# Performance work log

Measured on AMD Instinct MI355X. Metric: run time of the kernel, lower is better.

The kernel has to match this reference:

```python
import jax, jax.numpy as jnp
import numpy as np

B, S, IN, OUT = 4, 2048, 4096, 16384

def setup_inputs() -> dict:
    key = jax.random.key(0)
    k1, k2, k3, k4 = jax.random.split(key, 4)
    inp = jax.random.normal(k1, (B, S, IN), dtype=jnp.float16)
    # int8 quantized weights, stored [in_features, out_features] (pre-transposed)
    qweight = jax.random.randint(k2, (IN, OUT), -128, 128, dtype=jnp.int32).astype(jnp.int8)
    # per-output-channel dequant scales, small positive values typical of symmetric quant
    weight_scales = (jax.random.uniform(k3, (OUT,), dtype=jnp.float32) * 0.01 + 0.001).astype(jnp.float16)
    bias = jax.random.normal(k4, (OUT,), dtype=jnp.float16)
    return {"input": inp, "qweight": qweight, "weight_scales": weight_scales, "bias": bias}

def reference(input, qweight, weight_scales, bias):
    # w8_a16_gemm: dequantize int8 weight with per-column scale, then GEMM in fp16
    w = qweight.astype(jnp.float16) * weight_scales[None, :]        # [IN, OUT]
    out = jnp.einsum('bsi,io->bso', input, w)                        # [B, S, OUT]
    return out + bias
```

## Files before the change

### kernel.cpp

```cpp
#include <hip/hip_runtime.h>
#include <stdint.h>


typedef __bf16 bf16x8 __attribute__((ext_vector_type(8)));
typedef float  f32x4  __attribute__((ext_vector_type(4)));

#define M_TOT 8192
#define N_TOT 16384
#define K_TOT 4096
#define BM 256
#define BN 256
#define BK 64
#define NT (K_TOT / BK)
#define SLOT_ELEMS 16384

__device__ __forceinline__ void gload_lds16(const void* g, void* l) {
  __builtin_amdgcn_global_load_lds(
      (const __attribute__((address_space(1))) unsigned int*)g,
      (__attribute__((address_space(3))) unsigned int*)l,
      16, 0, 0);
}

__global__ void __launch_bounds__(256)
prep_kernel(const float* __restrict__ A, __bf16* __restrict__ Abf,
            const int* __restrict__ Q, __bf16* __restrict__ Bt) {
  __shared__ __bf16 t[64][72];
  const int tid = threadIdx.x;
  if (blockIdx.x < 16384) {
    const size_t i = ((size_t)blockIdx.x * 256 + tid) * 8;
    f32x4 lo = *(const f32x4*)(A + i);
    f32x4 hi = *(const f32x4*)(A + i + 4);
    bf16x8 v;
    #pragma unroll
    for (int j = 0; j < 4; ++j) {
      v[j]     = (__bf16)lo[j];
      v[j + 4] = (__bf16)hi[j];
    }
    *(bf16x8*)(Abf + i) = v;
  } else {
    const int bid = blockIdx.x - 16384;
    const int bk = bid & 63;
    const int bn = bid >> 6;
    const int k0 = bk * 64, n0 = bn * 64;
    const int tx = tid & 63;
    const int ty = tid >> 6;
    const int kb = ty * 16;
    int q[16];
    #pragma unroll
    for (int i = 0; i < 16; ++i)
      q[i] = Q[(size_t)(k0 + kb + i) * N_TOT + n0 + tx];
    bf16x8 v0, v1;
    #pragma unroll
    for (int i = 0; i < 8; ++i) {
      v0[i] = (__bf16)(float)q[i];
      v1[i] = (__bf16)(float)q[i + 8];
    }
    *(bf16x8*)&t[tx][kb]     = v0;
    *(bf16x8*)&t[tx][kb + 8] = v1;
    __syncthreads();
    const int nrow = tid >> 2;
    const int kc   = (tid & 3) * 16;
    bf16x8 w0 = *(const bf16x8*)&t[nrow][kc];
    bf16x8 w1 = *(const bf16x8*)&t[nrow][kc + 8];
    __bf16* dst = Bt + (size_t)(n0 + nrow) * K_TOT + k0 + kc;
    *(bf16x8*)(dst)     = w0;
    *(bf16x8*)(dst + 8) = w1;
  }
}

__global__ void __launch_bounds__(512, 2)
w8a16_gemm_ws(const __bf16* __restrict__ A,
              const __bf16* __restrict__ Bt,
              const float*  __restrict__ S,
              const float*  __restrict__ Bias,
              float*        __restrict__ O)
{
  extern __shared__ __bf16 lds[];
  __bf16* const aBase = lds;
  __bf16* const bBase = lds + 3 * SLOT_ELEMS;

  const int tid  = threadIdx.x;
  const int lane = tid & 63;
  const int wv   = tid >> 6;
  const int wm   = wv >> 2;
  const int wn   = wv & 3;
  const int rot  = (wv >> 2) << 1;

  const int bid = blockIdx.x;
  const int xcd = bid & 7;
  const int c   = bid >> 3;
  const int bx  = xcd * 8 + (c >> 5);
  const int by  = c & 31;
  const int m0  = by * BM;
  const int n0  = bx * BN;

  const int rr   = tid >> 3;
  const int cswz = (tid & 7) ^ (rr & 7);
  const __bf16* pa0 = A  + (size_t)(m0 + 0   + rr) * K_TOT + cswz * 8;
  const __bf16* pa1 = A  + (size_t)(m0 + 64  + rr) * K_TOT + cswz * 8;
  const __bf16* pa2 = A  + (size_t)(m0 + 128 + rr) * K_TOT + cswz * 8;
  const __bf16* pa3 = A  + (size_t)(m0 + 192 + rr) * K_TOT + cswz * 8;
  const __bf16* pb0 = Bt + (size_t)(n0 + 0   + rr) * K_TOT + cswz * 8;
  const __bf16* pb1 = Bt + (size_t)(n0 + 64  + rr) * K_TOT + cswz * 8;
  const __bf16* pb2 = Bt + (size_t)(n0 + 128 + rr) * K_TOT + cswz * 8;
  const __bf16* pb3 = Bt + (size_t)(n0 + 192 + rr) * K_TOT + cswz * 8;
  const int dA = tid * 8;

#define STAGE_A(dst) do {                                  \
    gload_lds16(pa0, (dst) + dA);                          \
    gload_lds16(pa1, (dst) + 4096  + dA);                  \
    gload_lds16(pa2, (dst) + 8192  + dA);                  \
    gload_lds16(pa3, (dst) + 12288 + dA);                  \
    pa0 += BK; pa1 += BK; pa2 += BK; pa3 += BK;            \
  } while (0)
#define STAGE_B(dst) do {                                  \
    gload_lds16(pb0, (dst) + dA);                          \
    gload_lds16(pb1, (dst) + 4096  + dA);                  \
    gload_lds16(pb2, (dst) + 8192  + dA);                  \
    gload_lds16(pb3, (dst) + 12288 + dA);                  \
    pb0 += BK; pb1 += BK; pb2 += BK; pb3 += BK;            \
  } while (0)

  const int l15     = lane & 15;
  const int quad    = lane >> 4;
  const int physA0  = quad ^ (l15 & 7);
  const int bRowOff = (wn * 64 + l15) * 64;

  f32x4 acc[8][4];
  #pragma unroll
  for (int i = 0; i < 8; ++i)
    #pragma unroll
    for (int j = 0; j < 4; ++j)
      acc[i][j] = {0.f, 0.f, 0.f, 0.f};

  bf16x8 b0[4][2], b1[4][2];

  STAGE_A(aBase);
  STAGE_B(bBase);
  STAGE_B(bBase + SLOT_ELEMS);
  STAGE_A(aBase + SLOT_ELEMS);
  asm volatile("s_waitcnt vmcnt(4)" ::: "memory");
  __builtin_amdgcn_s_barrier();

  #pragma unroll
  for (int ni = 0; ni < 4; ++ni)
    #pragma unroll
    for (int ks = 0; ks < 2; ++ks)
      b0[ni][ks] = *(const bf16x8*)(
          bBase + bRowOff + ni * 1024 + (physA0 ^ (ks << 2)) * 8);
  asm volatile("s_waitcnt lgkmcnt(0)" ::: "memory");
  __builtin_amdgcn_s_barrier();

  int csA = 0;
  int nsA = 2;

#define TILE_BODY(t, BCUR, BNXT, bStageLds, bReadLds) do {                  \
    if ((t) < NT - 1) { asm volatile("s_waitcnt vmcnt(4)" ::: "memory"); }  \
    else              { asm volatile("s_waitcnt vmcnt(0)" ::: "memory"); }  \
    asm volatile("s_waitcnt lgkmcnt(0)" ::: "memory");                      \
    __builtin_amdgcn_s_barrier();                                           \
    const __bf16* const aC_ = aBase + csA * SLOT_ELEMS;                     \
    __bf16* const aN_ = aBase + nsA * SLOT_ELEMS;                           \
    _Pragma("unroll")                                                       \
    for (int pp = 0; pp < 4; ++pp) {                                        \
      const int qq = (pp + rot) & 3;                                        \
      const __bf16* aQ = aC_ + (wm * 128 + qq * 32 + l15) * 64;             \
      bf16x8 aA[2][2];                                                      \
      _Pragma("unroll")                                                     \
      for (int i = 0; i < 2; ++i)                                           \
        _Pragma("unroll")                                                   \
        for (int ks = 0; ks < 2; ++ks)                                      \
          aA[i][ks] = *(const bf16x8*)(                                     \
              aQ + i * 1024 + (physA0 ^ (ks << 2)) * 8);                    \
      if ((t) + 1 < NT) {                                                   \
        BNXT[pp][0] = *(const bf16x8*)(                                     \
            (bReadLds) + bRowOff + pp * 1024 + physA0 * 8);                 \
        BNXT[pp][1] = *(const bf16x8*)(                                     \
            (bReadLds) + bRowOff + pp * 1024 + (physA0 ^ 4) * 8);           \
      }                                                                     \
      if (pp == 0 && (t) + 2 < NT) STAGE_B(bStageLds);                      \
      if (pp == 1 && (t) + 2 < NT) STAGE_A(aN_);                            \
      __builtin_amdgcn_s_setprio(1);                                        \
      _Pragma("unroll")                                                     \
      for (int i = 0; i < 2; ++i)                                           \
        _Pragma("unroll")                                                   \
        for (int ni = 0; ni < 4; ++ni)                                      \
          _Pragma("unroll")                                                 \
          for (int ks = 0; ks < 2; ++ks)                                    \
            acc[2 * pp + i][ni] = __builtin_amdgcn_mfma_f32_16x16x32_bf16(  \
                aA[i][ks], BCUR[ni][ks], acc[2 * pp + i][ni], 0, 0, 0);     \
      __builtin_amdgcn_s_setprio(0);                                        \
    }                                                                       \
    csA = (csA == 2) ? 0 : csA + 1;                                         \
    nsA = (nsA == 2) ? 0 : nsA + 1;                                         \
  } while (0)

  for (int tt = 0; tt < NT; tt += 2) {
    TILE_BODY(tt,     b0, b1, bBase,              bBase + SLOT_ELEMS);
    TILE_BODY(tt + 1, b1, b0, bBase + SLOT_ELEMS, bBase);
  }
#undef TILE_BODY
#undef STAGE_A
#undef STAGE_B

  const int colb = n0 + wn * 64 + l15;
  #pragma unroll
  for (int pp = 0; pp < 4; ++pp) {
    const int qq = (pp + rot) & 3;
    const int rowq = m0 + wm * 128 + qq * 32 + quad * 4;
    #pragma unroll
    for (int i = 0; i < 2; ++i) {
      const int rowb = rowq + i * 16;
      #pragma unroll
      for (int ni = 0; ni < 4; ++ni) {
        const int col = colb + ni * 16;
        const float sc = S[col];
        const float bb = Bias[col];
        f32x4 a = acc[2 * pp + i][ni];
        #pragma unroll
        for (int j = 0; j < 4; ++j)
          O[(size_t)(rowb + j) * N_TOT + col] = a[j] * sc + bb;
      }
    }
  }
}

#define FBM 128
#define FBN 128
#define FBK 32
#define BSTRIDE 40
__device__ __forceinline__ int swz_s(int row) {
  return (row & 3) ^ ((row >> 2) & 1);
}
__global__ void __launch_bounds__(256)
w8a16_gemm_fused(const float* __restrict__ A, const int* __restrict__ Q,
                 const float* __restrict__ S, const float* __restrict__ Bias,
                 float* __restrict__ O)
{
  __shared__ __bf16 a_lds[FBM * FBK];
  __shared__ __bf16 b_lds[FBN * BSTRIDE];
  const int tid = threadIdx.x, lane = tid & 63, wv = tid >> 6;
  const int bid = blockIdx.x;
  const int swz = (bid & 7) * 1024 + (bid >> 3);
  const int bx = swz >> 6, by = swz & 63;
  const int m0 = by * FBM, n0 = bx * FBN;
  const int mA0 = tid >> 2, mA1 = (256 + tid) >> 2;
  const int kcA = tid & 3;
  const int kp0 = kcA ^ swz_s(mA0), kp1 = kcA ^ swz_s(mA1);
  const float* pA0 = A + (size_t)(m0 + mA0) * K_TOT + kcA * 8;
  const float* pA1 = A + (size_t)(m0 + mA1) * K_TOT + kcA * 8;
  __bf16* dA0 = a_lds + mA0 * FBK + kp0 * 8;
  __bf16* dA1 = a_lds + mA1 * FBK + kp1 * 8;
  const int nB = tid & 127, kg = (tid >> 7) * 16;
  const int* pQ = Q + (size_t)kg * N_TOT + n0 + nB;
  __bf16* dB = b_lds + nB * BSTRIDE + kg;
  const int wr = (wv >> 1) * 64, wc = (wv & 1) * 64;
  const int r15 = lane & 15, kgrp = lane >> 4;
  const int selA = kgrp ^ swz_s(r15);
  const __bf16* aRd = a_lds + (wr + r15) * FBK + selA * 8;
  const __bf16* bRd = b_lds + (wc + r15) * BSTRIDE + kgrp * 8;
  f32x4 acc[4][4];
  #pragma unroll
  for (int i = 0; i < 4; ++i)
    #pragma unroll
    for (int j = 0; j < 4; ++j) acc[i][j] = {0.f, 0.f, 0.f, 0.f};
  for (int kt = 0; kt < K_TOT / FBK; ++kt) {
    f32x4 a0lo = *(const f32x4*)(pA0), a0hi = *(const f32x4*)(pA0 + 4);
    f32x4 a1lo = *(const f32x4*)(pA1), a1hi = *(const f32x4*)(pA1 + 4);
    pA0 += FBK; pA1 += FBK;
    bf16x8 a0, a1;
    #pragma unroll
    for (int i = 0; i < 4; ++i) {
      a0[i] = (__bf16)a0lo[i]; a0[i + 4] = (__bf16)a0hi[i];
      a1[i] = (__bf16)a1lo[i]; a1[i + 4] = (__bf16)a1hi[i];
    }
    int qv[16];
    #pragma unroll
    for (int i = 0; i < 16; ++i) qv[i] = pQ[(size_t)i * N_TOT];
    pQ += (size_t)FBK * N_TOT;
    bf16x8 v0, v1;
    #pragma unroll
    for (int i = 0; i < 8; ++i) { v0[i] = (__bf16)(float)qv[i]; v1[i] = (__bf16)(float)qv[i + 8]; }
    *(bf16x8*)dA0 = a0; *(bf16x8*)dA1 = a1;
    *(bf16x8*)(dB) = v0; *(bf16x8*)(dB + 8) = v1;
    __syncthreads();
    bf16x8 af[4], bfr[4];
    #pragma unroll
    for (int mi = 0; mi < 4; ++mi) af[mi] = *(const bf16x8*)(aRd + mi * 16 * FBK);
    #pragma unroll
    for (int ni = 0; ni < 4; ++ni) bfr[ni] = *(const bf16x8*)(bRd + ni * 16 * BSTRIDE);
    #pragma unroll
    for (int mi = 0; mi < 4; ++mi)
      #pragma unroll
      for (int ni = 0; ni < 4; ++ni)
        acc[mi][ni] = __builtin_amdgcn_mfma_f32_16x16x32_bf16(af[mi], bfr[ni], acc[mi][ni], 0, 0, 0);
    __syncthreads();
  }
  const int colb = n0 + wc + r15, rowb = m0 + wr + kgrp * 4;
  #pragma unroll
  for (int ni = 0; ni < 4; ++ni) {
    const int col = colb + ni * 16;
    const float sc = S[col], bb = Bias[col];
    #pragma unroll
    for (int mi = 0; mi < 4; ++mi) {
      const int row = rowb + mi * 16;
      f32x4 a = acc[mi][ni];
      #pragma unroll
      for (int j = 0; j < 4; ++j)
        O[(size_t)(row + j) * N_TOT + col] = a[j] * sc + bb;
    }
  }
}

extern "C" void kernel_launch(void* const* d_in, const int* in_sizes, int n_in,
                              void* d_out, int out_size, void* d_ws, size_t ws_size,
                              hipStream_t stream) {
  const float* A    = (const float*)d_in[0];
  const int*   Q    = (const int*)d_in[1];
  const float* S    = (const float*)d_in[2];
  const float* Bias = (const float*)d_in[3];
  float*       O    = (float*)d_out;

  const size_t A_BYTES = (size_t)M_TOT * K_TOT * 2;
  const size_t B_BYTES = (size_t)N_TOT * K_TOT * 2;
  const int    LDS_BYTES = 5 * SLOT_ELEMS * 2;

  if (ws_size >= A_BYTES + B_BYTES) {
    (void)hipFuncSetAttribute((const void*)&w8a16_gemm_ws,
                              hipFuncAttributeMaxDynamicSharedMemorySize,
                              LDS_BYTES);
    __bf16* Abf = (__bf16*)d_ws;
    __bf16* Bt  = (__bf16*)((char*)d_ws + A_BYTES);
    prep_kernel<<<dim3(32768), dim3(256), 0, stream>>>(A, Abf, Q, Bt);
    w8a16_gemm_ws<<<dim3(2048), dim3(512), LDS_BYTES, stream>>>(Abf, Bt, S, Bias, O);
  } else {
    w8a16_gemm_fused<<<dim3(8192), dim3(256), 0, stream>>>(A, Q, S, Bias, O);
  }
}
```

Before: 1.149 ms.

## Switch main GEMM loop from 16x16x32 to 32x32x16 bf16 MFMA tiles

Replaces the 16x16x32 MFMA instruction tiling with 32x32x16 MFMAs. Each wave now holds 4x2 f32x16 accumulators instead of 8x4 f32x4. The LDS fragment reads, the swizzle indexing and the epilogue row/column mapping are reworked to match the larger instruction's operand layout. The aim is fewer MFMA issues and fewer LDS reads per unit of work, in exchange for a more complex register layout and possibly different LDS bank-conflict behaviour.

```diff
diff --git a/kernel.cpp b/kernel.cpp
--- a/kernel.cpp
+++ b/kernel.cpp
@@ -4,6 +4,7 @@
 
 typedef __bf16 bf16x8 __attribute__((ext_vector_type(8)));
 typedef float  f32x4  __attribute__((ext_vector_type(4)));
+typedef float  f32x16 __attribute__((ext_vector_type(16)));
 
 #define M_TOT 8192
 #define N_TOT 16384
@@ -118,36 +119,38 @@
     gload_lds16(pb1, (dst) + 4096  + dA);                  \
     gload_lds16(pb2, (dst) + 8192  + dA);                  \
     gload_lds16(pb3, (dst) + 12288 + dA);                  \
-    pb0 += BK; pb1 += BK; pb2 += BK; pb3 += BK;            \
   } while (0)
-
-  const int l15     = lane & 15;
-  const int quad    = lane >> 4;
-  const int physA0  = quad ^ (l15 & 7);
-  const int bRowOff = (wn * 64 + l15) * 64;
-
-  f32x4 acc[8][4];
-  #pragma unroll
-  for (int i = 0; i < 8; ++i)
-    #pragma unroll
-    for (int j = 0; j < 4; ++j)
-      acc[i][j] = {0.f, 0.f, 0.f, 0.f};
-
-  bf16x8 b0[4][2], b1[4][2];
+#define ADV_B() do { pb0 += BK; pb1 += BK; pb2 += BK; pb3 += BK; } while (0)
+
+  const int l31   = lane & 31;
+  const int kq    = lane >> 5;
+  const int phys0 = kq ^ (l31 & 7);
+  const int bRowOff = (wn * 64 + l31) * 64;
+
+  f32x16 acc[4][2];
+  #pragma unroll
+  for (int i = 0; i < 4; ++i)
+    #pragma unroll
+    for (int j = 0; j < 2; ++j)
+      #pragma unroll
+      for (int r = 0; r < 16; ++r)
+        acc[i][j][r] = 0.f;
+
+  bf16x8 b0[2][4], b1[2][4];
 
   STAGE_A(aBase);
-  STAGE_B(bBase);
-  STAGE_B(bBase + SLOT_ELEMS);
+  STAGE_B(bBase);            ADV_B();
+  STAGE_B(bBase + SLOT_ELEMS); ADV_B();
   STAGE_A(aBase + SLOT_ELEMS);
   asm volatile("s_waitcnt vmcnt(4)" ::: "memory");
   __builtin_amdgcn_s_barrier();
 
   #pragma unroll
-  for (int ni = 0; ni < 4; ++ni)
-    #pragma unroll
-    for (int ks = 0; ks < 2; ++ks)
+  for (int ni = 0; ni < 2; ++ni)
+    #pragma unroll
+    for (int ks = 0; ks < 4; ++ks)
       b0[ni][ks] = *(const bf16x8*)(
-          bBase + bRowOff + ni * 1024 + (physA0 ^ (ks << 2)) * 8);
+          bBase + bRowOff + ni * 2048 + (((ks << 1) ^ phys0)) * 8);
   asm volatile("s_waitcnt lgkmcnt(0)" ::: "memory");
   __builtin_amdgcn_s_barrier();
 
@@ -164,31 +167,30 @@
     _Pragma("unroll")                                                       \
     for (int pp = 0; pp < 4; ++pp) {                                        \
       const int qq = (pp + rot) & 3;                                        \
-      const __bf16* aQ = aC_ + (wm * 128 + qq * 32 + l15) * 64;             \
-      bf16x8 aA[2][2];                                                      \
+      const __bf16* aQ = aC_ + (wm * 128 + qq * 32 + l31) * 64;             \
+      bf16x8 aA[4];                                                         \
       _Pragma("unroll")                                                     \
-      for (int i = 0; i < 2; ++i)                                           \
-        _Pragma("unroll")                                                   \
-        for (int ks = 0; ks < 2; ++ks)                                      \
-          aA[i][ks] = *(const bf16x8*)(                                     \
-              aQ + i * 1024 + (physA0 ^ (ks << 2)) * 8);                    \
+      for (int ks = 0; ks < 4; ++ks)                                        \
+        aA[ks] = *(const bf16x8*)(aQ + (((ks << 1) ^ phys0)) * 8);          \
       if ((t) + 1 < NT) {                                                   \
-        BNXT[pp][0] = *(const bf16x8*)(                                     \
-            (bReadLds) + bRowOff + pp * 1024 + physA0 * 8);                 \
-        BNXT[pp][1] = *(const bf16x8*)(                                     \
-            (bReadLds) + bRowOff + pp * 1024 + (physA0 ^ 4) * 8);           \
+        const int ni_ = pp >> 1;                                            \
+        const int ks_ = (pp & 1) << 1;                                      \
+        BNXT[ni_][ks_] = *(const bf16x8*)(                                  \
+            (bReadLds) + bRowOff + ni_ * 2048 +                             \
+            (((ks_ << 1) ^ phys0)) * 8);                                    \
+        BNXT[ni_][ks_ + 1] = *(const bf16x8*)(                              \
+            (bReadLds) + bRowOff + ni_ * 2048 +                             \
+            ((((ks_ + 1) << 1) ^ phys0)) * 8);                              \
       }                                                                     \
-      if (pp == 0 && (t) + 2 < NT) STAGE_B(bStageLds);                      \
+      if (pp == 0 && (t) + 2 < NT) { STAGE_B(bStageLds); ADV_B(); }         \
       if (pp == 1 && (t) + 2 < NT) STAGE_A(aN_);                            \
       __builtin_amdgcn_s_setprio(1);                                        \
       _Pragma("unroll")                                                     \
-      for (int i = 0; i < 2; ++i)                                           \
+      for (int ni = 0; ni < 2; ++ni)                                        \
         _Pragma("unroll")                                                   \
-        for (int ni = 0; ni < 4; ++ni)                                      \
-          _Pragma("unroll")                                                 \
-          for (int ks = 0; ks < 2; ++ks)                                    \
-            acc[2 * pp + i][ni] = __builtin_amdgcn_mfma_f32_16x16x32_bf16(  \
-                aA[i][ks], BCUR[ni][ks], acc[2 * pp + i][ni], 0, 0, 0);     \
+        for (int ks = 0; ks < 4; ++ks)                                      \
+          acc[pp][ni] = __builtin_amdgcn_mfma_f32_32x32x16_bf16(            \
+              aA[ks], BCUR[ni][ks], acc[pp][ni], 0, 0, 0);                  \
       __builtin_amdgcn_s_setprio(0);                                        \
     }                                                                       \
     csA = (csA == 2) ? 0 : csA + 1;                                         \
@@ -202,24 +204,21 @@
 #undef TILE_BODY
 #undef STAGE_A
 #undef STAGE_B
-
-  const int colb = n0 + wn * 64 + l15;
+#undef ADV_B
+
   #pragma unroll
   for (int pp = 0; pp < 4; ++pp) {
     const int qq = (pp + rot) & 3;
-    const int rowq = m0 + wm * 128 + qq * 32 + quad * 4;
-    #pragma unroll
-    for (int i = 0; i < 2; ++i) {
-      const int rowb = rowq + i * 16;
+    const int rowq = m0 + wm * 128 + qq * 32 + kq * 4;
+    #pragma unroll
+    for (int ni = 0; ni < 2; ++ni) {
+      const int col = n0 + wn * 64 + ni * 32 + l31;
+      const float sc = S[col];
+      const float bb = Bias[col];
       #pragma unroll
-      for (int ni = 0; ni < 4; ++ni) {
-        const int col = colb + ni * 16;
-        const float sc = S[col];
-        const float bb = Bias[col];
-        f32x4 a = acc[2 * pp + i][ni];
-        #pragma unroll
-        for (int j = 0; j < 4; ++j)
-          O[(size_t)(rowb + j) * N_TOT + col] = a[j] * sc + bb;
+      for (int reg = 0; reg < 16; ++reg) {
+        const int row = rowq + (reg & 3) + ((reg >> 2) << 3);
+        O[(size_t)row * N_TOT + col] = acc[pp][ni][reg] * sc + bb;
       }
     }
   }
```

Result: slower. 1.176 ms (+2.3%).
